# Kernel tuning notes

Hardware: AMD Instinct MI355X
Metric: run time of the kernel (lower is better)

## Reference

```python
import jax, jax.numpy as jnp
import numpy as np

# TT config: input_dimension=2048, output_multiplier=4, rank=16
# top_ranks    = [8,2,2,2,2,2,2,2,2]  (prod = 2048)
# bottom_ranks = [8,2,2,2,2,2,2,2,2]  (prod = 2048)
# core shapes (top, bottom, left, right): left/right are TT bond ranks.
CORE_SHAPES = [(8, 8, 1, 16)] + [(2, 2, 16, 16)] * 7 + [(2, 2, 16, 1)]


def setup_inputs() -> dict:
    key = jax.random.key(0)
    ks = jax.random.split(key, 10)
    inp = {"x": jax.random.normal(ks[0], (4, 2048, 2048), dtype=jnp.float32)}
    for i, s in enumerate(CORE_SHAPES):
        inp[f"p{i}"] = jax.random.normal(ks[i + 1], s, dtype=jnp.float32)
    return inp


def _tt_apply(x, ps):
    # x: [B, S, D] with D = prod(top_ranks) = 2048
    B, S, D = x.shape
    T = B * S
    # Normalize every core to (top, bottom, left_bond_in, right_bond_out).
    # Original einsum: '... abcdefghi, ajs, bkst, cltu, dmuv, envw, fowx, gpxy, hqzy, irz -> ... jklmnopqr'
    # Core 7 ('hqzy') has swapped bonds: its 4th dim (y) is the incoming bond
    # from core 6 and its 3rd dim (z) is the outgoing bond into core 8 ('irz').
    cores = list(ps[:7]) + [jnp.transpose(ps[7], (0, 1, 3, 2)), ps[8]]
    # core 0 is used as p0[:, :, 0, :] in the original; its left dim is 1 so
    # keeping the singleton left axis is identical math.
    y = x.reshape(T, 1, 1, D)  # [T, out_so_far=1, bond=1, remaining_top=D]
    J, M = 1, D
    for g in cores:
        tk, bk, lk, rk = g.shape
        y = y.reshape(T, J, lk, tk, M // tk)
        # contract incoming bond l and current top index a with the core
        y = jnp.einsum('tjlam,ablr->tjbrm', y, g)
        J *= bk
        M //= tk
        y = y.reshape(T, J, rk, M)
    # final: rk == 1, M == 1 -> [T, J] with J = prod(bottom_ranks) = 2048
    return y.reshape(B, S, J)


def reference(x, p0, p1, p2, p3, p4, p5, p6, p7, p8):
    return _tt_apply(x, (p0, p1, p2, p3, p4, p5, p6, p7, p8))
```

## Files before the change

kernel.cpp:

```cpp
#include <hip/hip_runtime.h>
#include <stdint.h>

typedef unsigned short u16;
typedef __bf16 bf16x8 __attribute__((ext_vector_type(8)));
typedef float f32x16 __attribute__((ext_vector_type(16)));
typedef u16 u16x8 __attribute__((ext_vector_type(8)));

__device__ __forceinline__ u16 f2bf(float f) {
  uint32_t u = __float_as_uint(f);
  u += 0x7fffu + ((u >> 16) & 1u);
  return (u16)(u >> 16);
}

__global__ __launch_bounds__(256) void build_lr_kernel(
    const float* __restrict__ p0, const float* __restrict__ p1,
    const float* __restrict__ p2, const float* __restrict__ p3,
    const float* __restrict__ p4, const float* __restrict__ p5,
    const float* __restrict__ p6, const float* __restrict__ p7,
    const float* __restrict__ p8, float* __restrict__ L4, float* __restrict__ R) {
  __shared__ float sA[16384];
  __shared__ float sB[4096];
  const int tid = threadIdx.x;
  if (blockIdx.x < 16) {
    for (int i = tid; i < 1024; i += 256) sA[i] = p0[i];
    __syncthreads();
    for (int i = tid; i < 4096; i += 256) {
      int r = i & 15, t = i >> 4;
      int Bb = t & 15, Aa = t >> 4;
      int a = Aa & 1, A = Aa >> 1, b = Bb & 1, B = Bb >> 1;
      const float* srow = sA + (A * 8 + B) * 16;
      const float* g = p1 + ((a * 2 + b) * 16) * 16 + r;
      float s = 0.f;
#pragma unroll
      for (int l = 0; l < 16; l++) s += srow[l] * g[l * 16];
      sB[i] = s;
    }
    __syncthreads();
    for (int i = tid; i < 16384; i += 256) {
      int r = i & 15, t = i >> 4;
      int Bb = t & 31, Aa = t >> 5;
      int a = Aa & 1, A = Aa >> 1, b = Bb & 1, B = Bb >> 1;
      const float* srow = sB + (A * 16 + B) * 16;
      const float* g = p2 + ((a * 2 + b) * 16) * 16 + r;
      float s = 0.f;
#pragma unroll
      for (int l = 0; l < 16; l++) s += srow[l] * g[l * 16];
      sA[i] = s;
    }
    __syncthreads();
    int gi = blockIdx.x * 256 + tid;
    int b3 = gi & 1, a3 = (gi >> 1) & 1;
    int B2 = (gi >> 2) & 31, A2 = gi >> 7;
    const float* srow = sA + (A2 * 32 + B2) * 16;
    const float* g3 = p3 + ((a3 * 2 + b3) * 16) * 16;
    float tmp[16];
#pragma unroll
    for (int r3 = 0; r3 < 16; r3++) {
      float s = 0.f;
#pragma unroll
      for (int r2 = 0; r2 < 16; r2++) s += srow[r2] * g3[r2 * 16 + r3];
      tmp[r3] = s;
    }
#pragma unroll
    for (int ab = 0; ab < 4; ab++) {
      int a4 = ab >> 1, b4 = ab & 1;
      const float* g4 = p4 + (ab * 16) * 16;
      int AL = A2 * 4 + a3 * 2 + a4;
      int BL = B2 * 4 + b3 * 2 + b4;
      float* drow = L4 + (AL * 128 + BL) * 16;
#pragma unroll
      for (int r4 = 0; r4 < 16; r4++) {
        float s = 0.f;
#pragma unroll
        for (int r3 = 0; r3 < 16; r3++) s += tmp[r3] * g4[r3 * 16 + r4];
        drow[r4] = s;
      }
    }
  } else {
    for (int i = tid; i < 64; i += 256) sA[i] = p8[i];
    __syncthreads();
    for (int i = tid; i < 256; i += 256) {
      int rl = i & 15, t = i >> 4;
      int Bt = t & 3, At = t >> 2;
      int a = At >> 1, Ap = At & 1, b = Bt >> 1, Bp = Bt & 1;
      const float* srow = sA + (Ap * 2 + Bp) * 16;
      const float* g = p7 + ((a * 2 + b) * 16) * 16 + rl;
      float s = 0.f;
#pragma unroll
      for (int rk = 0; rk < 16; rk++) s += srow[rk] * g[rk * 16];
      sB[i] = s;
    }
    __syncthreads();
    for (int i = tid; i < 1024; i += 256) {
      int rl = i & 15, t = i >> 4;
      int Bt = t & 7, At = t >> 3;
      int a = At >> 2, Ap = At & 3, b = Bt >> 2, Bp = Bt & 3;
      const float* srow = sB + (Ap * 4 + Bp) * 16;
      const float* g = p6 + (((a * 2 + b) * 16) + rl) * 16;
      float s = 0.f;
#pragma unroll
      for (int rk = 0; rk < 16; rk++) s += srow[rk] * g[rk];
      sA[i] = s;
    }
    __syncthreads();
    for (int i = tid; i < 4096; i += 256) {
      int rl = i & 15, t = i >> 4;
      int Bt = t & 15, At = t >> 4;
      int a = At >> 3, Ap = At & 7, b = Bt >> 3, Bp = Bt & 7;
      const float* srow = sA + (Ap * 8 + Bp) * 16;
      const float* g = p5 + (((a * 2 + b) * 16) + rl) * 16;
      float s = 0.f;
#pragma unroll
      for (int rk = 0; rk < 16; rk++) s += srow[rk] * g[rk];
      R[i] = s;
    }
  }
}

__global__ __launch_bounds__(256) void merge_kernel(const float* __restrict__ L4,
                                                    const float* __restrict__ R,
                                                    u16* __restrict__ Wt) {
  int t = blockIdx.x * 256 + threadIdx.x;
  int e = t * 8;
  int Af = e & 2047;
  int Bf = e >> 11;
  const float* lrow = L4 + ((Af >> 4) * 128 + (Bf >> 4)) * 16;
  float lv[16];
#pragma unroll
  for (int r = 0; r < 16; r++) lv[r] = lrow[r];
  const float* rbase = R + (Bf & 15) * 16;
  u16x8 o;
#pragma unroll
  for (int j = 0; j < 8; j++) {
    const float* rrow = rbase + ((Af + j) & 15) * 256;
    float s = 0.f;
#pragma unroll
    for (int r = 0; r < 16; r++) s += lv[r] * rrow[r];
    o[j] = f2bf(s);
  }
  *(u16x8*)(Wt + (size_t)Bf * 2048 + Af) = o;
}

__global__ __launch_bounds__(256) void cast_x_kernel(const float* __restrict__ x,
                                                     u16* __restrict__ xb) {
  size_t i = ((size_t)blockIdx.x * 256 + threadIdx.x) * 8;
  float4 u = *(const float4*)(x + i);
  float4 v = *(const float4*)(x + i + 4);
  u16x8 o;
  o[0] = f2bf(u.x); o[1] = f2bf(u.y); o[2] = f2bf(u.z); o[3] = f2bf(u.w);
  o[4] = f2bf(v.x); o[5] = f2bf(v.y); o[6] = f2bf(v.z); o[7] = f2bf(v.w);
  *(u16x8*)(xb + i) = o;
}

__global__ __launch_bounds__(256, 2) void gemm_kernel(const u16* __restrict__ A,
                                                      const u16* __restrict__ B,
                                                      float* __restrict__ C) {
  __shared__ u16 As[256 * 32];
  __shared__ u16 Bs[128 * 32];
  const int tid = threadIdx.x;
  const int lane = tid & 63;
  const int w = tid >> 6;
  const int m0 = blockIdx.y * 256;
  const int n0 = blockIdx.x * 128;
  const int wm = w * 64;
  const int r32 = lane & 31;
  const int half = lane >> 5;
  const int lrow = lane >> 2;
  const int oct = (lane & 3) ^ ((lrow >> 1) & 3);

  const u16* gaA = A + (size_t)(m0 + w * 16 + lrow) * 2048 + oct * 8;
  const u16* gaB = B + (size_t)(n0 + w * 16 + lrow) * 2048 + oct * 8;

  const int sw = (r32 >> 1) & 3;

  f32x16 acc[2][4] = {};

  for (int k0 = 0; k0 < 2048; k0 += 32) {
#pragma unroll
    for (int q = 0; q < 4; q++)
      __builtin_amdgcn_global_load_lds(
          (const __attribute__((address_space(1))) void*)(gaA + k0 + (size_t)q * 64 * 2048),
          (__attribute__((address_space(3))) void*)(As + (q * 4 + w) * 512), 16, 0, 0);
#pragma unroll
    for (int q = 0; q < 2; q++)
      __builtin_amdgcn_global_load_lds(
          (const __attribute__((address_space(1))) void*)(gaB + k0 + (size_t)q * 64 * 2048),
          (__attribute__((address_space(3))) void*)(Bs + (q * 4 + w) * 512), 16, 0, 0);
    __syncthreads();
    bf16x8 af[2][2], bv[4][2];
#pragma unroll
    for (int mt = 0; mt < 2; mt++)
#pragma unroll
      for (int ks = 0; ks < 2; ks++)
        af[mt][ks] = *(const bf16x8*)(As + (wm + mt * 32 + r32) * 32 +
                                      ((ks * 2 + half) ^ sw) * 8);
#pragma unroll
    for (int nt = 0; nt < 4; nt++)
#pragma unroll
      for (int ks = 0; ks < 2; ks++)
        bv[nt][ks] = *(const bf16x8*)(Bs + (nt * 32 + r32) * 32 +
                                      ((ks * 2 + half) ^ sw) * 8);
#pragma unroll
    for (int ks = 0; ks < 2; ks++)
#pragma unroll
      for (int mt = 0; mt < 2; mt++)
#pragma unroll
        for (int nt = 0; nt < 4; nt++)
          acc[mt][nt] = __builtin_amdgcn_mfma_f32_32x32x16_bf16(af[mt][ks], bv[nt][ks], acc[mt][nt], 0, 0, 0);
    __syncthreads();
  }
#pragma unroll
  for (int mt = 0; mt < 2; mt++) {
#pragma unroll
    for (int nt = 0; nt < 4; nt++) {
      size_t cbase = (size_t)(m0 + wm + mt * 32 + 4 * half) * 2048 + (n0 + nt * 32 + r32);
#pragma unroll
      for (int reg = 0; reg < 16; reg++) {
        int row = (reg & 3) + 8 * (reg >> 2);
        __builtin_nontemporal_store(acc[mt][nt][reg], C + cbase + (size_t)row * 2048);
      }
    }
  }
}

extern "C" void kernel_launch(void* const* d_in, const int* in_sizes, int n_in,
                              void* d_out, int out_size, void* d_ws, size_t ws_size,
                              hipStream_t stream) {
  const float* x = (const float*)d_in[0];
  const float* p0 = (const float*)d_in[1];
  const float* p1 = (const float*)d_in[2];
  const float* p2 = (const float*)d_in[3];
  const float* p3 = (const float*)d_in[4];
  const float* p4 = (const float*)d_in[5];
  const float* p5 = (const float*)d_in[6];
  const float* p6 = (const float*)d_in[7];
  const float* p7 = (const float*)d_in[8];
  const float* p8 = (const float*)d_in[9];
  char* ws = (char*)d_ws;
  u16* xbf = (u16*)ws;
  u16* Wt = (u16*)(ws + 33554432);
  float* L4 = (float*)(ws + 41943040);
  float* R = (float*)(ws + 42991616);

  build_lr_kernel<<<17, 256, 0, stream>>>(p0, p1, p2, p3, p4, p5, p6, p7, p8, L4, R);
  merge_kernel<<<2048, 256, 0, stream>>>(L4, R, Wt);
  cast_x_kernel<<<8192, 256, 0, stream>>>(x, xbf);
  gemm_kernel<<<dim3(16, 32), 256, 0, stream>>>(xbf, Wt, (float*)d_out);
}
```

Before: 269.9 us.

## Double-buffer LDS tiles in bf16 GEMM to overlap global loads with MFMA

The GEMM main loop now uses two LDS buffers for the A and B tiles. It issues the async global-to-LDS loads for the next K-step before computing on the current one. Explicit s_waitcnt on vmcnt and raw s_barrier calls replace the two __syncthreads per iteration, so memory latency can hide behind the MFMA work. The cost is twice the LDS per block, which could limit occupancy, and the hand-coded waitcnt immediates are fragile.

```diff
diff --git a/kernel.cpp b/kernel.cpp
--- a/kernel.cpp
+++ b/kernel.cpp
@@ -155,8 +155,8 @@
 __global__ __launch_bounds__(256, 2) void gemm_kernel(const u16* __restrict__ A,
                                                       const u16* __restrict__ B,
                                                       float* __restrict__ C) {
-  __shared__ u16 As[256 * 32];
-  __shared__ u16 Bs[128 * 32];
+  __shared__ u16 As[2][256 * 32];
+  __shared__ u16 Bs[2][128 * 32];
   const int tid = threadIdx.x;
   const int lane = tid & 63;
   const int w = tid >> 6;
@@ -173,42 +173,54 @@
 
   const int sw = (r32 >> 1) & 3;
 
+#define STAGE(buf, k0)                                                                     \
+  do {                                                                                     \
+    _Pragma("unroll") for (int q = 0; q < 4; q++)                                          \
+        __builtin_amdgcn_global_load_lds(                                                  \
+            (const __attribute__((address_space(1))) void*)(gaA + (k0) + (size_t)q * 64 * 2048), \
+            (__attribute__((address_space(3))) void*)(&As[buf][(q * 4 + w) * 512]), 16, 0, 0);   \
+    _Pragma("unroll") for (int q = 0; q < 2; q++)                                          \
+        __builtin_amdgcn_global_load_lds(                                                  \
+            (const __attribute__((address_space(1))) void*)(gaB + (k0) + (size_t)q * 64 * 2048), \
+            (__attribute__((address_space(3))) void*)(&Bs[buf][(q * 4 + w) * 512]), 16, 0, 0);   \
+  } while (0)
+
+#define COMPUTE(buf)                                                                       \
+  do {                                                                                     \
+    bf16x8 af[2][2], bv[4][2];                                                             \
+    _Pragma("unroll") for (int mt = 0; mt < 2; mt++)                                       \
+        _Pragma("unroll") for (int ks = 0; ks < 2; ks++)                                   \
+            af[mt][ks] = *(const bf16x8*)(&As[buf][(wm + mt * 32 + r32) * 32 +             \
+                                                   ((ks * 2 + half) ^ sw) * 8]);           \
+    _Pragma("unroll") for (int nt = 0; nt < 4; nt++)                                       \
+        _Pragma("unroll") for (int ks = 0; ks < 2; ks++)                                   \
+            bv[nt][ks] = *(const bf16x8*)(&Bs[buf][(nt * 32 + r32) * 32 +                  \
+                                                   ((ks * 2 + half) ^ sw) * 8]);           \
+    _Pragma("unroll") for (int ks = 0; ks < 2; ks++)                                       \
+        _Pragma("unroll") for (int mt = 0; mt < 2; mt++)                                   \
+            _Pragma("unroll") for (int nt = 0; nt < 4; nt++)                               \
+                acc[mt][nt] = __builtin_amdgcn_mfma_f32_32x32x16_bf16(                     \
+                    af[mt][ks], bv[nt][ks], acc[mt][nt], 0, 0, 0);                         \
+  } while (0)
+
   f32x16 acc[2][4] = {};
 
-  for (int k0 = 0; k0 < 2048; k0 += 32) {
-#pragma unroll
-    for (int q = 0; q < 4; q++)
-      __builtin_amdgcn_global_load_lds(
-          (const __attribute__((address_space(1))) void*)(gaA + k0 + (size_t)q * 64 * 2048),
-          (__attribute__((address_space(3))) void*)(As + (q * 4 + w) * 512), 16, 0, 0);
-#pragma unroll
-    for (int q = 0; q < 2; q++)
-      __builtin_amdgcn_global_load_lds(
-          (const __attribute__((address_space(1))) void*)(gaB + k0 + (size_t)q * 64 * 2048),
-          (__attribute__((address_space(3))) void*)(Bs + (q * 4 + w) * 512), 16, 0, 0);
-    __syncthreads();
-    bf16x8 af[2][2], bv[4][2];
-#pragma unroll
-    for (int mt = 0; mt < 2; mt++)
-#pragma unroll
-      for (int ks = 0; ks < 2; ks++)
-        af[mt][ks] = *(const bf16x8*)(As + (wm + mt * 32 + r32) * 32 +
-                                      ((ks * 2 + half) ^ sw) * 8);
-#pragma unroll
-    for (int nt = 0; nt < 4; nt++)
-#pragma unroll
-      for (int ks = 0; ks < 2; ks++)
-        bv[nt][ks] = *(const bf16x8*)(Bs + (nt * 32 + r32) * 32 +
-                                      ((ks * 2 + half) ^ sw) * 8);
-#pragma unroll
-    for (int ks = 0; ks < 2; ks++)
-#pragma unroll
-      for (int mt = 0; mt < 2; mt++)
-#pragma unroll
-        for (int nt = 0; nt < 4; nt++)
-          acc[mt][nt] = __builtin_amdgcn_mfma_f32_32x32x16_bf16(af[mt][ks], bv[nt][ks], acc[mt][nt], 0, 0, 0);
-    __syncthreads();
-  }
+  STAGE(0, 0);
+  for (int ki = 0; ki < 63; ki++) {
+    const int cur = ki & 1;
+    __builtin_amdgcn_s_barrier();
+    STAGE(cur ^ 1, (ki + 1) * 32);
+    __builtin_amdgcn_s_waitcnt(0x0F76);
+    __builtin_amdgcn_s_barrier();
+    COMPUTE(cur);
+  }
+  __builtin_amdgcn_s_waitcnt(0x0F70);
+  __builtin_amdgcn_s_barrier();
+  COMPUTE(1);
+
+#undef STAGE
+#undef COMPUTE
+
 #pragma unroll
   for (int mt = 0; mt < 2; mt++) {
 #pragma unroll
```

After: 277.6 us. 2.9% more time.
